# Kernel optimization log

Hardware: AMD Instinct MI355X
Metric: run time of the kernel (lower is better)

## Reference

```python
import jax, jax.numpy as jnp
import numpy as np


def _rodrigues(axis, theta):
    # axis [..., 3] (unit), theta [...] -> rotation matrices [..., 3, 3]
    ax, ay, az = axis[..., 0], axis[..., 1], axis[..., 2]
    z = jnp.zeros_like(ax)
    K = jnp.stack([jnp.stack([z, -az, ay], -1),
                   jnp.stack([az, z, -ax], -1),
                   jnp.stack([-ay, ax, z], -1)], -2)
    s = jnp.sin(theta)[..., None, None]
    c = jnp.cos(theta)[..., None, None]
    I = jnp.eye(3, dtype=axis.dtype)
    return I + s * K + (1.0 - c) * (K @ K)


def setup_inputs() -> dict:
    B, L, NS = 8192, 16, 8
    key = jax.random.key(0)
    k = jax.random.split(key, 7)

    def unit(v):
        return v / jnp.linalg.norm(v, axis=-1, keepdims=True)

    q = 0.5 * jax.random.normal(k[0], (B, L), dtype=jnp.float32)
    joint_axes = unit(jax.random.normal(k[1], (L, 3), dtype=jnp.float32))
    # fixed per-joint URDF transforms: small random rotation + translation
    fa = unit(jax.random.normal(k[2], (L, 3), dtype=jnp.float32))
    fth = jax.random.uniform(k[3], (L,), minval=-0.3, maxval=0.3, dtype=jnp.float32)
    fixed_rot = _rodrigues(fa, fth)
    fixed_trans = 0.15 * jax.random.normal(k[4], (L, 3), dtype=jnp.float32)
    centers = 0.05 * jax.random.normal(k[5], (L, NS, 3), dtype=jnp.float32)
    radii = 0.03 + 0.05 * jax.random.uniform(k[6], (L, NS), dtype=jnp.float32)
    link_spheres = jnp.concatenate([centers, radii[..., None]], axis=-1)
    # self-collision ignore: adjacent links (and self) are ignored, like typical URDF configs
    idx = jnp.arange(L)
    collision_mask = jnp.abs(idx[:, None] - idx[None, :]) > 1  # True = pair is checked
    return {"q": q, "fixed_rot": fixed_rot, "fixed_trans": fixed_trans,
            "joint_axes": joint_axes, "link_spheres": link_spheres,
            "collision_mask": collision_mask}


def reference(q, fixed_rot, fixed_trans, joint_axes, link_spheres, collision_mask):
    B, L = q.shape
    NS = link_spheres.shape[1]

    # ---- forward kinematics: serial tree walk (parent -> child), one revolute joint per link
    def step(carry, inp):
        Rp, tp = carry                      # parent world pose [B,3,3],[B,3]
        frot, ftrans, axis, qi = inp        # [3,3],[3],[3],[B]
        Rj = _rodrigues(jnp.broadcast_to(axis, (B, 3)), qi)          # [B,3,3]
        R = jnp.einsum('bij,jk,bkl->bil', Rp, frot, Rj)
        t = tp + jnp.einsum('bij,j->bi', Rp, ftrans)
        return (R, t), (R, t)

    R0 = jnp.broadcast_to(jnp.eye(3, dtype=q.dtype), (B, 3, 3))
    t0 = jnp.zeros((B, 3), dtype=q.dtype)
    _, (Rs, ts) = jax.lax.scan(step, (R0, t0), (fixed_rot, fixed_trans, joint_axes, q.T))
    # Rs [L,B,3,3], ts [L,B,3]

    # ---- transform collision spheres to world frame: [B,L,NS,3]
    centers_w = jnp.einsum('lbij,lsj->blsi', Rs, link_spheres[..., :3]) \
        + ts.transpose(1, 0, 2)[:, :, None, :]

    # ---- pairwise sphere penetration distance (r_i + r_j - ||c_i - c_j||)
    N = L * NS
    cn = centers_w.reshape(B, N, 3)
    sq = jnp.sum(cn * cn, axis=-1)                                   # [B,N]
    d2 = sq[:, :, None] + sq[:, None, :] - 2.0 * jnp.einsum('bnd,bmd->bnm', cn, cn)
    dist = jnp.sqrt(jnp.maximum(d2, 1e-12))                          # [B,N,N]
    r = link_spheres[..., 3].reshape(N)
    pen = r[None, :, None] + r[None, None, :] - dist                 # [B,N,N]

    # per link-pair max over sphere pairs -> [B,L,L]
    pair = jnp.max(pen.reshape(B, L, NS, L, NS), axis=(2, 4))
    # ignored pairs / diagonal get -100 (matches dist buffer init in find_link_distance)
    pair = jnp.where(collision_mask[None, :, :], pair, jnp.float32(-100.0))
    link_dist = jnp.max(pair, axis=-1)                               # [B,L]
    return link_dist
```

## Files before the change

### kernel.cpp

```cpp
#include <hip/hip_runtime.h>

typedef float v2f __attribute__((ext_vector_type(2)));

template<int CTRL>
__device__ __forceinline__ float dppmov(float x) {
    return __builtin_bit_cast(float,
        __builtin_amdgcn_update_dpp(0, __builtin_bit_cast(int, x),
                                    CTRL, 0xf, 0xf, true));
}
#define DPP_XOR1  0xB1
#define DPP_XOR2  0x4E
#define DPP_XOR8  0x128
#define DPP_SHR(d) (0x110 | (d))

__device__ __forceinline__ void pen2(const float4& r0, const float4& r1,
                                     const float4& c,
                                     float& m0, float& m1, float& mj)
{
    v2f dx = (v2f){r0.x, r1.x} - c.x;
    v2f dy = (v2f){r0.y, r1.y} - c.y;
    v2f dz = (v2f){r0.z, r1.z} - c.z;
    v2f d2 = dx * dx;
    d2 = __builtin_elementwise_fma(dy, dy, d2);
    d2 = __builtin_elementwise_fma(dz, dz, d2);
    float s0 = __builtin_amdgcn_sqrtf(d2.x);
    float s1 = __builtin_amdgcn_sqrtf(d2.y);
    v2f pen = ((v2f){r0.w, r1.w} + c.w) - (v2f){s0, s1};
    m0 = fmaxf(m0, pen.x);
    m1 = fmaxf(m1, pen.y);
    mj = fmaxf(fmaxf(mj, pen.x), pen.y);
}

__device__ __forceinline__ void pen1(const float4& r, const float4& c,
                                     float& mi, float& mj)
{
    float dx = r.x - c.x, dy = r.y - c.y, dz = r.z - c.z;
    float d2 = fmaf(dx, dx, fmaf(dy, dy, dz * dz));
    float p  = r.w + c.w - __builtin_amdgcn_sqrtf(d2);
    mi = fmaxf(mi, p);
    mj = fmaxf(mj, p);
}

__global__ __launch_bounds__(256) void fused_kernel(
    const float* __restrict__ q,
    const float* __restrict__ frot,
    const float* __restrict__ ftrans,
    const float* __restrict__ axes,
    const float* __restrict__ spheres,
    float* __restrict__ out,
    int B)
{
    __shared__ float4 sph[4][16 * 9];
    const int t    = threadIdx.x;
    const int w    = t >> 6;
    const int lane = t & 63;
    int b = blockIdx.x * 4 + w;
    const bool alive = (b < B);
    if (!alive) b = B - 1;

    const int l = lane & 15;
    const int g = lane >> 4;

    const float qv = q[(size_t)b * 16 + l];
    const float s = __sinf(qv), c = __cosf(qv), oc = 1.0f - c;
    const float ax = axes[3*l+0], ay = axes[3*l+1], az = axes[3*l+2];

    const float F00=frot[9*l+0], F01=frot[9*l+1], F02=frot[9*l+2];
    const float F10=frot[9*l+3], F11=frot[9*l+4], F12=frot[9*l+5];
    const float F20=frot[9*l+6], F21=frot[9*l+7], F22=frot[9*l+8];

    float R00,R01,R02,R10,R11,R12,R20,R21,R22;
    {
        float u0 = fmaf(F01,az, -F02*ay);
        float u1 = fmaf(F02,ax, -F00*az);
        float u2 = fmaf(F00,ay, -F01*ax);
        float v0 = fmaf(u1,az, -u2*ay);
        float v1 = fmaf(u2,ax, -u0*az);
        float v2 = fmaf(u0,ay, -u1*ax);
        R00 = fmaf(oc,v0, fmaf(s,u0, F00));
        R01 = fmaf(oc,v1, fmaf(s,u1, F01));
        R02 = fmaf(oc,v2, fmaf(s,u2, F02));

        u0 = fmaf(F11,az, -F12*ay);
        u1 = fmaf(F12,ax, -F10*az);
        u2 = fmaf(F10,ay, -F11*ax);
        v0 = fmaf(u1,az, -u2*ay);
        v1 = fmaf(u2,ax, -u0*az);
        v2 = fmaf(u0,ay, -u1*ax);
        R10 = fmaf(oc,v0, fmaf(s,u0, F10));
        R11 = fmaf(oc,v1, fmaf(s,u1, F11));
        R12 = fmaf(oc,v2, fmaf(s,u2, F12));

        u0 = fmaf(F21,az, -F22*ay);
        u1 = fmaf(F22,ax, -F20*az);
        u2 = fmaf(F20,ay, -F21*ax);
        v0 = fmaf(u1,az, -u2*ay);
        v1 = fmaf(u2,ax, -u0*az);
        v2 = fmaf(u0,ay, -u1*ax);
        R20 = fmaf(oc,v0, fmaf(s,u0, F20));
        R21 = fmaf(oc,v1, fmaf(s,u1, F21));
        R22 = fmaf(oc,v2, fmaf(s,u2, F22));
    }
    float t0 = ftrans[3*l+0], t1 = ftrans[3*l+1], t2 = ftrans[3*l+2];

    #define SCAN_STEP(D, CTRL)                                                  \
    {                                                                           \
        float P00 = dppmov<CTRL>(R00), P01 = dppmov<CTRL>(R01), P02 = dppmov<CTRL>(R02); \
        float P10 = dppmov<CTRL>(R10), P11 = dppmov<CTRL>(R11), P12 = dppmov<CTRL>(R12); \
        float P20 = dppmov<CTRL>(R20), P21 = dppmov<CTRL>(R21), P22 = dppmov<CTRL>(R22); \
        float pt0 = dppmov<CTRL>(t0),  pt1 = dppmov<CTRL>(t1),  pt2 = dppmov<CTRL>(t2);  \
        if (l >= (D)) {                                                         \
            float n00 = fmaf(P00,R00, fmaf(P01,R10, P02*R20));                  \
            float n01 = fmaf(P00,R01, fmaf(P01,R11, P02*R21));                  \
            float n02 = fmaf(P00,R02, fmaf(P01,R12, P02*R22));                  \
            float n10 = fmaf(P10,R00, fmaf(P11,R10, P12*R20));                  \
            float n11 = fmaf(P10,R01, fmaf(P11,R11, P12*R21));                  \
            float n12 = fmaf(P10,R02, fmaf(P11,R12, P12*R22));                  \
            float n20 = fmaf(P20,R00, fmaf(P21,R10, P22*R20));                  \
            float n21 = fmaf(P20,R01, fmaf(P21,R11, P22*R21));                  \
            float n22 = fmaf(P20,R02, fmaf(P21,R12, P22*R22));                  \
            float nt0 = fmaf(P00,t0, fmaf(P01,t1, fmaf(P02,t2, pt0)));          \
            float nt1 = fmaf(P10,t0, fmaf(P11,t1, fmaf(P12,t2, pt1)));          \
            float nt2 = fmaf(P20,t0, fmaf(P21,t1, fmaf(P22,t2, pt2)));          \
            R00=n00; R01=n01; R02=n02;                                          \
            R10=n10; R11=n11; R12=n12;                                          \
            R20=n20; R21=n21; R22=n22;                                          \
            t0=nt0; t1=nt1; t2=nt2;                                             \
        }                                                                       \
    }
    SCAN_STEP(1, DPP_SHR(1))
    SCAN_STEP(2, DPP_SHR(2))
    SCAN_STEP(4, DPP_SHR(4))
    SCAN_STEP(8, DPP_SHR(8))
    #undef SCAN_STEP

    #pragma unroll
    for (int k = 0; k < 2; ++k) {
        const int sp = g * 2 + k;
        float4 cs = reinterpret_cast<const float4*>(spheres)[l*8 + sp];
        float wx = fmaf(R00,cs.x, fmaf(R01,cs.y, fmaf(R02,cs.z, t0)));
        float wy = fmaf(R10,cs.x, fmaf(R11,cs.y, fmaf(R12,cs.z, t1)));
        float wz = fmaf(R20,cs.x, fmaf(R21,cs.y, fmaf(R22,cs.z, t2)));
        sph[w][l*9 + sp] = make_float4(wx, wy, wz, cs.w);
    }
    asm volatile("s_waitcnt lgkmcnt(0)" ::: "memory");

    const float4* S = sph[w];
    const int sr = lane >> 3;
    const int sc = lane & 7;

    float m[16];
    #pragma unroll
    for (int k = 0; k < 16; ++k) m[k] = -100.0f;

    {
        float4 cs[7];
        #pragma unroll
        for (int j = 2; j <= 8; ++j) cs[j-2] = S[j*9 + sc];

        float4 r0 = S[0*9 + sr], r1 = S[1*9 + sr];
        pen1(r0, cs[0], m[0], m[2]);
        #pragma unroll
        for (int j = 3; j <= 8; ++j) pen2(r0, r1, cs[j-2], m[0], m[1], m[j]);

        r0 = S[2*9 + sr]; r1 = S[3*9 + sr];
        pen1(r0, cs[2], m[2], m[4]);
        #pragma unroll
        for (int j = 5; j <= 8; ++j) pen2(r0, r1, cs[j-2], m[2], m[3], m[j]);

        r0 = S[4*9 + sr]; r1 = S[5*9 + sr];
        pen1(r0, cs[4], m[4], m[6]);
        #pragma unroll
        for (int j = 7; j <= 8; ++j) pen2(r0, r1, cs[j-2], m[4], m[5], m[j]);

        r0 = S[6*9 + sr];
        pen1(r0, cs[6], m[6], m[8]);
    }

    {
        float4 cs[7];
        #pragma unroll
        for (int j = 9; j <= 15; ++j) cs[j-9] = S[j*9 + sc];

        #pragma unroll
        for (int k = 0; k < 4; ++k) {
            float4 r0 = S[(2*k)*9 + sr], r1 = S[(2*k+1)*9 + sr];
            #pragma unroll
            for (int j = 9; j <= 15; ++j) pen2(r0, r1, cs[j-9], m[2*k], m[2*k+1], m[j]);
        }

        float4 r0 = S[8*9 + sr], r1 = S[9*9 + sr];
        pen1(r0, cs[1], m[8], m[10]);
        #pragma unroll
        for (int j = 11; j <= 15; ++j) pen2(r0, r1, cs[j-9], m[8], m[9], m[j]);

        r0 = S[10*9 + sr]; r1 = S[11*9 + sr];
        pen1(r0, cs[3], m[10], m[12]);
        #pragma unroll
        for (int j = 13; j <= 15; ++j) pen2(r0, r1, cs[j-9], m[10], m[11], m[j]);

        r0 = S[12*9 + sr]; r1 = S[13*9 + sr];
        pen1(r0, cs[5], m[12], m[14]);
        pen2(r0, r1, cs[6], m[12], m[13], m[15]);
    }

    {
        int bit0 = lane & 1;
        #pragma unroll
        for (int k = 0; k < 8; ++k) {
            float send = bit0 ? m[k] : m[k+8];
            float recv = dppmov<DPP_XOR1>(send);
            m[k] = fmaxf(bit0 ? m[k+8] : m[k], recv);
        }
        int bit1 = (lane >> 1) & 1;
        #pragma unroll
        for (int k = 0; k < 4; ++k) {
            float send = bit1 ? m[k] : m[k+4];
            float recv = dppmov<DPP_XOR2>(send);
            m[k] = fmaxf(bit1 ? m[k+4] : m[k], recv);
        }
        int bit2 = (lane >> 2) & 1;
        #pragma unroll
        for (int k = 0; k < 2; ++k) {
            float send = bit2 ? m[k] : m[k+2];
            float recv = __shfl_xor(send, 4, 64);
            m[k] = fmaxf(bit2 ? m[k+2] : m[k], recv);
        }
        int bit3 = (lane >> 3) & 1;
        {
            float send = bit3 ? m[0] : m[1];
            float recv = dppmov<DPP_XOR8>(send);
            m[0] = fmaxf(bit3 ? m[1] : m[0], recv);
        }
        float v = m[0];
        v = fmaxf(v, __shfl_xor(v, 16, 64));
        v = fmaxf(v, __shfl_xor(v, 32, 64));
        m[0] = v;
    }

    if (alive && lane < 16) {
        int k = ((lane & 1) << 3) | ((lane & 2) << 1) | ((lane & 4) >> 1) | ((lane & 8) >> 3);
        out[(size_t)b * 16 + k] = m[0];
    }
}

extern "C" void kernel_launch(void* const* d_in, const int* in_sizes, int n_in,
                              void* d_out, int out_size, void* d_ws, size_t ws_size,
                              hipStream_t stream) {
    const float* q      = (const float*)d_in[0];
    const float* frot   = (const float*)d_in[1];
    const float* ftrans = (const float*)d_in[2];
    const float* axes   = (const float*)d_in[3];
    const float* sphere = (const float*)d_in[4];
    float* out = (float*)d_out;

    const int B = in_sizes[0] / 16;
    const int blocks = (B + 3) / 4;
    fused_kernel<<<dim3(blocks), dim3(256), 0, stream>>>(
        q, frot, ftrans, axes, sphere, out, B);
}
```

Measured before the change: 23.32 us.

## Process two batch items per wavefront with half-wave pairwise sphere tiling

Each 64-lane wavefront now handles two batch elements, one per 32-lane half, and each lane computes a 1x2 tile of sphere pairs instead of 2x1. Each lane also writes four world-frame spheres instead of two. This halves the block count and drops one cross-lane shuffle stage from the reduction. The pairwise loops are regenerated uniformly, with packed v2f column operands loaded as scalar LDS reads, and launch bounds now request 4 blocks. The per-lane pairwise work doubles, traded against fewer waves and less shared FK overhead per batch item.

```diff
diff --git a/kernel.cpp b/kernel.cpp
--- a/kernel.cpp
+++ b/kernel.cpp
@@ -13,35 +13,23 @@
 #define DPP_XOR8  0x128
 #define DPP_SHR(d) (0x110 | (d))
 
-__device__ __forceinline__ void pen2(const float4& r0, const float4& r1,
-                                     const float4& c,
-                                     float& m0, float& m1, float& mj)
+__device__ __forceinline__ void pen2p(const float4& rs,
+                                      v2f cx, v2f cy, v2f cz, v2f cw,
+                                      float& mi, float& mj)
 {
-    v2f dx = (v2f){r0.x, r1.x} - c.x;
-    v2f dy = (v2f){r0.y, r1.y} - c.y;
-    v2f dz = (v2f){r0.z, r1.z} - c.z;
+    v2f dx = cx - rs.x;
+    v2f dy = cy - rs.y;
+    v2f dz = cz - rs.z;
     v2f d2 = dx * dx;
     d2 = __builtin_elementwise_fma(dy, dy, d2);
     d2 = __builtin_elementwise_fma(dz, dz, d2);
-    float s0 = __builtin_amdgcn_sqrtf(d2.x);
-    float s1 = __builtin_amdgcn_sqrtf(d2.y);
-    v2f pen = ((v2f){r0.w, r1.w} + c.w) - (v2f){s0, s1};
-    m0 = fmaxf(m0, pen.x);
-    m1 = fmaxf(m1, pen.y);
+    v2f pen = (cw + rs.w) - (v2f){__builtin_amdgcn_sqrtf(d2.x),
+                                  __builtin_amdgcn_sqrtf(d2.y)};
+    mi = fmaxf(fmaxf(mi, pen.x), pen.y);
     mj = fmaxf(fmaxf(mj, pen.x), pen.y);
 }
 
-__device__ __forceinline__ void pen1(const float4& r, const float4& c,
-                                     float& mi, float& mj)
-{
-    float dx = r.x - c.x, dy = r.y - c.y, dz = r.z - c.z;
-    float d2 = fmaf(dx, dx, fmaf(dy, dy, dz * dz));
-    float p  = r.w + c.w - __builtin_amdgcn_sqrtf(d2);
-    mi = fmaxf(mi, p);
-    mj = fmaxf(mj, p);
-}
-
-__global__ __launch_bounds__(256) void fused_kernel(
+__global__ __launch_bounds__(256, 4) void fused_kernel(
     const float* __restrict__ q,
     const float* __restrict__ frot,
     const float* __restrict__ ftrans,
@@ -50,16 +38,17 @@
     float* __restrict__ out,
     int B)
 {
-    __shared__ float4 sph[4][16 * 9];
+    __shared__ float4 sph[4][2][16 * 9];
     const int t    = threadIdx.x;
     const int w    = t >> 6;
     const int lane = t & 63;
-    int b = blockIdx.x * 4 + w;
+    const int h    = lane >> 5;
+    int b = blockIdx.x * 8 + w * 2 + h;
     const bool alive = (b < B);
     if (!alive) b = B - 1;
 
     const int l = lane & 15;
-    const int g = lane >> 4;
+    const int g = (lane >> 4) & 1;
 
     const float qv = q[(size_t)b * 16 + l];
     const float s = __sinf(qv), c = __cosf(qv), oc = 1.0f - c;
@@ -135,74 +124,65 @@
     #undef SCAN_STEP
 
     #pragma unroll
-    for (int k = 0; k < 2; ++k) {
-        const int sp = g * 2 + k;
+    for (int k = 0; k < 4; ++k) {
+        const int sp = g * 4 + k;
         float4 cs = reinterpret_cast<const float4*>(spheres)[l*8 + sp];
         float wx = fmaf(R00,cs.x, fmaf(R01,cs.y, fmaf(R02,cs.z, t0)));
         float wy = fmaf(R10,cs.x, fmaf(R11,cs.y, fmaf(R12,cs.z, t1)));
         float wz = fmaf(R20,cs.x, fmaf(R21,cs.y, fmaf(R22,cs.z, t2)));
-        sph[w][l*9 + sp] = make_float4(wx, wy, wz, cs.w);
+        sph[w][h][l*9 + sp] = make_float4(wx, wy, wz, cs.w);
     }
     asm volatile("s_waitcnt lgkmcnt(0)" ::: "memory");
 
-    const float4* S = sph[w];
-    const int sr = lane >> 3;
-    const int sc = lane & 7;
+    const float4* S  = sph[w][h];
+    const float*  Sf = reinterpret_cast<const float*>(S);
+    const int L   = lane & 31;
+    const int sr  = L >> 2;
+    const int sc2 = L & 3;
 
     float m[16];
     #pragma unroll
     for (int k = 0; k < 16; ++k) m[k] = -100.0f;
 
-    {
-        float4 cs[7];
-        #pragma unroll
-        for (int j = 2; j <= 8; ++j) cs[j-2] = S[j*9 + sc];
-
-        float4 r0 = S[0*9 + sr], r1 = S[1*9 + sr];
-        pen1(r0, cs[0], m[0], m[2]);
-        #pragma unroll
-        for (int j = 3; j <= 8; ++j) pen2(r0, r1, cs[j-2], m[0], m[1], m[j]);
-
-        r0 = S[2*9 + sr]; r1 = S[3*9 + sr];
-        pen1(r0, cs[2], m[2], m[4]);
-        #pragma unroll
-        for (int j = 5; j <= 8; ++j) pen2(r0, r1, cs[j-2], m[2], m[3], m[j]);
-
-        r0 = S[4*9 + sr]; r1 = S[5*9 + sr];
-        pen1(r0, cs[4], m[4], m[6]);
-        #pragma unroll
-        for (int j = 7; j <= 8; ++j) pen2(r0, r1, cs[j-2], m[4], m[5], m[j]);
-
-        r0 = S[6*9 + sr];
-        pen1(r0, cs[6], m[6], m[8]);
-    }
-
-    {
-        float4 cs[7];
-        #pragma unroll
-        for (int j = 9; j <= 15; ++j) cs[j-9] = S[j*9 + sc];
-
-        #pragma unroll
-        for (int k = 0; k < 4; ++k) {
-            float4 r0 = S[(2*k)*9 + sr], r1 = S[(2*k+1)*9 + sr];
+    #define FILL_CS(jj, j)                                                      \
+    {                                                                           \
+        const int bd = (j)*36 + sc2*4;                                          \
+        cx[jj] = (v2f){Sf[bd+0], Sf[bd+16]};                                    \
+        cy[jj] = (v2f){Sf[bd+1], Sf[bd+17]};                                    \
+        cz[jj] = (v2f){Sf[bd+2], Sf[bd+18]};                                    \
+        cw[jj] = (v2f){Sf[bd+3], Sf[bd+19]};                                    \
+    }
+
+    {
+        v2f cx[7], cy[7], cz[7], cw[7];
+        #pragma unroll
+        for (int j = 2; j <= 8; ++j) FILL_CS(j-2, j)
+
+        #pragma unroll
+        for (int i = 0; i <= 6; ++i) {
+            float4 rs = S[i*9 + sr];
             #pragma unroll
-            for (int j = 9; j <= 15; ++j) pen2(r0, r1, cs[j-9], m[2*k], m[2*k+1], m[j]);
-        }
-
-        float4 r0 = S[8*9 + sr], r1 = S[9*9 + sr];
-        pen1(r0, cs[1], m[8], m[10]);
-        #pragma unroll
-        for (int j = 11; j <= 15; ++j) pen2(r0, r1, cs[j-9], m[8], m[9], m[j]);
-
-        r0 = S[10*9 + sr]; r1 = S[11*9 + sr];
-        pen1(r0, cs[3], m[10], m[12]);
-        #pragma unroll
-        for (int j = 13; j <= 15; ++j) pen2(r0, r1, cs[j-9], m[10], m[11], m[j]);
-
-        r0 = S[12*9 + sr]; r1 = S[13*9 + sr];
-        pen1(r0, cs[5], m[12], m[14]);
-        pen2(r0, r1, cs[6], m[12], m[13], m[15]);
-    }
+            for (int j = i + 2; j <= 8; ++j)
+                pen2p(rs, cx[j-2], cy[j-2], cz[j-2], cw[j-2], m[i], m[j]);
+        }
+    }
+    {
+        v2f cx[7], cy[7], cz[7], cw[7];
+        #pragma unroll
+        for (int j = 9; j <= 15; ++j) FILL_CS(j-9, j)
+
+        #pragma unroll
+        for (int i = 0; i <= 13; ++i) {
+            float4 rs = S[i*9 + sr];
+            const int j0 = (i + 2 > 9) ? (i + 2) : 9;
+            #pragma unroll
+            for (int j = 9; j <= 15; ++j) {
+                if (j < j0) continue;
+                pen2p(rs, cx[j-9], cy[j-9], cz[j-9], cw[j-9], m[i], m[j]);
+            }
+        }
+    }
+    #undef FILL_CS
 
     {
         int bit0 = lane & 1;
@@ -234,11 +214,10 @@
         }
         float v = m[0];
         v = fmaxf(v, __shfl_xor(v, 16, 64));
-        v = fmaxf(v, __shfl_xor(v, 32, 64));
         m[0] = v;
     }
 
-    if (alive && lane < 16) {
+    if (alive && (lane & 16) == 0) {
         int k = ((lane & 1) << 3) | ((lane & 2) << 1) | ((lane & 4) >> 1) | ((lane & 8) >> 3);
         out[(size_t)b * 16 + k] = m[0];
     }
@@ -255,7 +234,7 @@
     float* out = (float*)d_out;
 
     const int B = in_sizes[0] / 16;
-    const int blocks = (B + 3) / 4;
+    const int blocks = (B + 7) / 8;
     fused_kernel<<<dim3(blocks), dim3(256), 0, stream>>>(
         q, frot, ftrans, axes, sphere, out, B);
 }
```

Measured after the change: 20.56 us. 1.13x faster.
